# Kernel tuning notes

Hardware: AMD Instinct MI355X
Metric: run time of the kernel (lower is better)

## Reference

```python
import jax, jax.numpy as jnp
import numpy as np

BS, S, D, H, HS, HSEL, L = 32, 512, 512, 8, 2, 4, 6
DK = D // H  # 64
HD = H - HS  # dynamic heads


def setup_inputs() -> dict:
    key = jax.random.key(0)
    ks = jax.random.split(key, 10)
    w = lambda k, shape: jax.random.normal(k, shape, dtype=jnp.float32) * 0.02
    return {
        'q_embed_data': jax.random.normal(ks[0], (BS, S, D), jnp.float32),
        'qa_embed_data': jax.random.normal(ks[1], (BS, S, D), jnp.float32),
        # stacked per-layer params (torch Linear convention: W[out,in], y = x@W.T+b)
        'Wq': w(ks[2], (L, D, D)), 'bq': jnp.zeros((L, D), jnp.float32),
        'Wv': w(ks[3], (L, D, D)), 'bv': jnp.zeros((L, D), jnp.float32),
        'Wg': w(ks[4], (L, HD, D)),                      # routing gate, no bias
        'Wo': w(ks[5], (L, D, D)), 'bo': jnp.zeros((L, D), jnp.float32),
        'ln1_g': jnp.ones((L, D), jnp.float32), 'ln1_b': jnp.zeros((L, D), jnp.float32),
        'W1': w(ks[6], (L, D, D)), 'b1': jnp.zeros((L, D), jnp.float32),
        'W2': w(ks[7], (L, D, D)), 'b2': jnp.zeros((L, D), jnp.float32),
        'ln2_g': jnp.ones((L, D), jnp.float32), 'ln2_b': jnp.zeros((L, D), jnp.float32),
    }


def _layer_norm(x, g, b):
    m = x.mean(-1, keepdims=True)
    v = ((x - m) ** 2).mean(-1, keepdims=True)
    return (x - m) * jax.lax.rsqrt(v + 1e-5) * g + b


def _moh_attention(xq, xv, Wq, bq, Wv, bv, Wg, Wo, bo, strict):
    bs, s, d = xq.shape
    q = xq @ Wq.T + bq            # kq_same=True: k = q projection
    v = xv @ Wv.T + bv
    qh = q.reshape(bs, s, H, DK).transpose(0, 2, 1, 3)   # [b,h,s,dk]
    vh = v.reshape(bs, s, H, DK).transpose(0, 2, 1, 3)
    scores = jnp.einsum('bhqd,bhkd->bhqk', qh, qh) / jnp.sqrt(jnp.float32(DK))
    # mask==1 -> causal incl. diag; mask==0 -> strictly causal
    allow = jnp.tril(jnp.ones((s, s), bool), k=-1 if strict else 0)
    scores = jnp.where(allow, scores, jnp.float32(-1e9))
    # pad-zero shift: first query row replaced by zeros -> uniform attention
    scores = scores.at[:, :, 0, :].set(0.0)
    # per-token top-k head routing over dynamic heads
    gates = jax.nn.softmax(q.reshape(bs * s, D) @ Wg.T, axis=-1)  # [bs*s, HD]
    _, idx = jax.lax.top_k(gates, HSEL)
    dmask = jnp.zeros_like(gates).at[jnp.arange(bs * s)[:, None], idx].set(1.0)
    dyn = (gates * dmask).reshape(bs, s, HD)
    routing = jnp.concatenate([jnp.ones((bs, s, HS), gates.dtype), dyn], -1).mean(1)  # [b,H]
    attn = jax.nn.softmax(scores, axis=-1)
    ctx = jnp.einsum('bhqk,bhkd->bhqd', attn, vh) * routing[:, :, None, None]
    out = ctx.transpose(0, 2, 1, 3).reshape(bs, s, D) @ Wo.T + bo
    f = dmask.sum(0)
    P = gates.mean(0)
    balance = jnp.sum((f / (f.sum() + 1e-5)) * (P / (P.sum() + 1e-5)))
    return out, balance


def reference(q_embed_data, qa_embed_data, Wq, bq, Wv, bv, Wg, Wo, bo,
              ln1_g, ln1_b, W1, b1, W2, b2, ln2_g, ln2_b):
    def layer(i, xq, xv, strict):
        a, bl = _moh_attention(xq, xv, Wq[i], bq[i], Wv[i], bv[i], Wg[i], Wo[i], bo[i], strict)
        x = _layer_norm(xq + a, ln1_g[i], ln1_b[i])
        ffn = jax.nn.relu(x @ W1[i].T + b1[i]) @ W2[i].T + b2[i]
        return _layer_norm(x + ffn, ln2_g[i], ln2_b[i]), bl

    y = qa_embed_data
    x = q_embed_data
    # blocks_1: self-attention on y, mask=1
    y, _ = layer(0, y, y, False)
    y, _ = layer(1, y, y, False)
    # blocks_2: alternate mask=1 self-attn / mask=0 cross-attn (values=y)
    x, _ = layer(2, x, x, False)
    x, bl = layer(3, x, y, True)
    x, _ = layer(4, x, x, False)
    x, bl = layer(5, x, y, True)
    return (x, bl)
```

## Files before the change

kernel.cpp:

```cpp
#include <hip/hip_runtime.h>
#include <cstdint>

#define BSZ 32
#define SEQ 512
#define DM  512
#define NH  8
#define DK  64
#define HS_ 2
#define HD_ 6
#define NL  6
#define MROWS (BSZ*SEQ)
#define QVLD 1024
#define SCL 0.18033688011112043f

typedef unsigned short bf16_t;
typedef __attribute__((ext_vector_type(4))) float f32x4;
typedef __attribute__((ext_vector_type(8))) short bf16x8;
typedef __attribute__((ext_vector_type(8))) unsigned short u16x8;

#define DEV static __device__ __forceinline__

DEV float bf2f(bf16_t b) {
  unsigned int u = ((unsigned int)b) << 16;
  float f; __builtin_memcpy(&f, &u, 4); return f;
}
DEV bf16_t f2b(float f) {
  unsigned int u; __builtin_memcpy(&u, &f, 4);
  unsigned int r = (u + 0x7fffu + ((u >> 16) & 1u)) >> 16;
  return (bf16_t)r;
}
DEV void unp2(unsigned int w, float& a, float& b) {
  unsigned int ua = w << 16, ub = w & 0xffff0000u;
  __builtin_memcpy(&a, &ua, 4); __builtin_memcpy(&b, &ub, 4);
}
DEV unsigned cvtpk(float lo, float hi) {
  unsigned r;
  asm("v_cvt_pk_bf16_f32 %0, %1, %2" : "=v"(r) : "v"(lo), "v"(hi));
  return r;
}

DEV void gload_lds16(const bf16_t* g, bf16_t* l) {
  __builtin_amdgcn_global_load_lds(
      (const __attribute__((address_space(1))) void*)g,
      (__attribute__((address_space(3))) void*)l, 16, 0, 0);
}

DEV bf16x8 scale_q(bf16x8 v) {
  u16x8 u;
  __builtin_memcpy(&u, &v, 16);
  unsigned w[4];
#pragma unroll
  for (int e = 0; e < 4; ++e)
    w[e] = cvtpk(bf2f(u[2 * e]) * SCL, bf2f(u[2 * e + 1]) * SCL);
  bf16x8 r;
  __builtin_memcpy(&r, w, 16);
  return r;
}

__global__ __launch_bounds__(256) void f2b2_kernel(
    const float* __restrict__ s0, const float* __restrict__ s1,
    bf16_t* __restrict__ d0, bf16_t* __restrict__ d1) {
  const float* s = blockIdx.y ? s1 : s0;
  bf16_t* d = blockIdx.y ? d1 : d0;
  const int i = blockIdx.x * 256 + threadIdx.x;
  float4 v = reinterpret_cast<const float4*>(s)[i];
  ushort4 o;
  o.x = f2b(v.x); o.y = f2b(v.y); o.z = f2b(v.z); o.w = f2b(v.w);
  reinterpret_cast<ushort4*>(d)[i] = o;
}

__global__ __launch_bounds__(256) void f2bw_kernel(
    const float* __restrict__ s0, const float* __restrict__ s1,
    const float* __restrict__ s2, const float* __restrict__ s3,
    const float* __restrict__ s4, bf16_t* __restrict__ dst) {
  const float* srcs[5] = {s0, s1, s2, s3, s4};
  const float* s = srcs[blockIdx.y];
  bf16_t* d = dst + (size_t)blockIdx.y * ((size_t)NL * DM * DM);
  const int i = blockIdx.x * 256 + threadIdx.x;
  float4 v = reinterpret_cast<const float4*>(s)[i];
  ushort4 o;
  o.x = f2b(v.x); o.y = f2b(v.y); o.z = f2b(v.z); o.w = f2b(v.w);
  reinterpret_cast<ushort4*>(d)[i] = o;
}

__global__ __launch_bounds__(256) void gemm_qv(
    const bf16_t* __restrict__ A0, const bf16_t* __restrict__ A1,
    const bf16_t* __restrict__ W0, const bf16_t* __restrict__ W1,
    const float* __restrict__ b0, const float* __restrict__ b1,
    bf16_t* __restrict__ Yb) {
  const int K = 512;
  const int lin = blockIdx.y * 8 + blockIdx.x;
  const int swz = (lin & 7) * 128 + (lin >> 3);
  const int bn = swz & 7, bm = swz >> 3;
  const int tid = threadIdx.x, wid = tid >> 6, lane = tid & 63;
  const int wr = wid >> 1, wc = wid & 1;
  __shared__ __align__(16) bf16_t As[128 * 64];
  __shared__ __align__(16) bf16_t Bs[128 * 64];

  const bool hi = bn >= 4;
  const bf16_t* Asel = hi ? A1 : A0;
  const bf16_t* Wsel = hi ? (W1 - (size_t)512 * K) : W0;
  const float* bsel = hi ? (b1 - 512) : b0;

  f32x4 acc[4][4];
#pragma unroll
  for (int m = 0; m < 4; ++m)
#pragma unroll
    for (int n = 0; n < 4; ++n) acc[m][n] = f32x4{0.f, 0.f, 0.f, 0.f};

  const int lrow = lane & 15, lko = (lane >> 4) * 8;
  const int sr = wid * 8 + (lane >> 3), scol = (lane & 7) * 8;
  const size_t arow0 = (size_t)bm * 128, brow0 = (size_t)bn * 128;

  for (int k0 = 0; k0 < K; k0 += 64) {
#pragma unroll
    for (int i = 0; i < 4; ++i) {
      gload_lds16(Asel + (arow0 + i * 32 + sr) * K + k0 + scol, &As[(i * 4 + wid) * 512]);
      gload_lds16(Wsel + (brow0 + i * 32 + sr) * K + k0 + scol, &Bs[(i * 4 + wid) * 512]);
    }
    __syncthreads();
    bf16x8 af[4][2], bw[4][2];
#pragma unroll
    for (int m = 0; m < 4; ++m)
#pragma unroll
      for (int ks = 0; ks < 2; ++ks)
        af[m][ks] = *reinterpret_cast<const bf16x8*>(
            &As[(wr * 64 + m * 16 + lrow) * 64 + ks * 32 + lko]);
#pragma unroll
    for (int n = 0; n < 4; ++n)
#pragma unroll
      for (int ks = 0; ks < 2; ++ks)
        bw[n][ks] = *reinterpret_cast<const bf16x8*>(
            &Bs[(wc * 64 + n * 16 + lrow) * 64 + ks * 32 + lko]);
    __builtin_amdgcn_s_setprio(1);
#pragma unroll
    for (int ks = 0; ks < 2; ++ks)
#pragma unroll
      for (int m = 0; m < 4; ++m)
#pragma unroll
        for (int n = 0; n < 4; ++n)
          acc[m][n] = __builtin_amdgcn_mfma_f32_16x16x32_bf16(af[m][ks], bw[n][ks], acc[m][n], 0, 0, 0);
    __builtin_amdgcn_s_setprio(0);
    __syncthreads();
  }

  const int r0 = bm * 128 + wr * 64 + (lane >> 4) * 4;
  const int c0 = bn * 128 + wc * 64 + lrow;
#pragma unroll
  for (int n = 0; n < 4; ++n) {
    const int col = c0 + n * 16;
    const float bc = bsel[col];
#pragma unroll
    for (int m = 0; m < 4; ++m)
#pragma unroll
      for (int j = 0; j < 4; ++j)
        Yb[(size_t)(r0 + m * 16 + j) * QVLD + col] = f2b(acc[m][n][j] + bc);
  }
}

template <bool RELU>
__global__ __launch_bounds__(256) void gemm_n512(
    const bf16_t* __restrict__ A, const bf16_t* __restrict__ W,
    const float* __restrict__ bias, bf16_t* __restrict__ Yb) {
  const int K = 512;
  const int lin = blockIdx.y * 4 + blockIdx.x;
  const int swz = (lin & 7) * 128 + (lin >> 3);
  const int bn = swz & 3, bm = swz >> 2;
  const int tid = threadIdx.x, wid = tid >> 6, lane = tid & 63;
  const int wr = wid >> 1, wc = wid & 1;
  __shared__ __align__(16) bf16_t As[64 * 64];
  __shared__ __align__(16) bf16_t Bs[128 * 64];

  f32x4 acc[2][4];
#pragma unroll
  for (int m = 0; m < 2; ++m)
#pragma unroll
    for (int n = 0; n < 4; ++n) acc[m][n] = f32x4{0.f, 0.f, 0.f, 0.f};

  const int lrow = lane & 15, lko = (lane >> 4) * 8;
  const int sr = wid * 8 + (lane >> 3), scol = (lane & 7) * 8;
  const size_t arow0 = (size_t)bm * 64, brow0 = (size_t)bn * 128;

  for (int k0 = 0; k0 < K; k0 += 64) {
#pragma unroll
    for (int i = 0; i < 2; ++i)
      gload_lds16(A + (arow0 + i * 32 + sr) * K + k0 + scol, &As[(i * 4 + wid) * 512]);
#pragma unroll
    for (int i = 0; i < 4; ++i)
      gload_lds16(W + (brow0 + i * 32 + sr) * K + k0 + scol, &Bs[(i * 4 + wid) * 512]);
    __syncthreads();
    bf16x8 af[2][2], bw[4][2];
#pragma unroll
    for (int m = 0; m < 2; ++m)
#pragma unroll
      for (int ks = 0; ks < 2; ++ks)
        af[m][ks] = *reinterpret_cast<const bf16x8*>(
            &As[(wr * 32 + m * 16 + lrow) * 64 + ks * 32 + lko]);
#pragma unroll
    for (int n = 0; n < 4; ++n)
#pragma unroll
      for (int ks = 0; ks < 2; ++ks)
        bw[n][ks] = *reinterpret_cast<const bf16x8*>(
            &Bs[(wc * 64 + n * 16 + lrow) * 64 + ks * 32 + lko]);
    __builtin_amdgcn_s_setprio(1);
#pragma unroll
    for (int ks = 0; ks < 2; ++ks)
#pragma unroll
      for (int m = 0; m < 2; ++m)
#pragma unroll
        for (int n = 0; n < 4; ++n)
          acc[m][n] = __builtin_amdgcn_mfma_f32_16x16x32_bf16(af[m][ks], bw[n][ks], acc[m][n], 0, 0, 0);
    __builtin_amdgcn_s_setprio(0);
    __syncthreads();
  }

  const int r0 = bm * 64 + wr * 32 + (lane >> 4) * 4;
  const int c0 = bn * 128 + wc * 64 + lrow;
#pragma unroll
  for (int n = 0; n < 4; ++n) {
    const int col = c0 + n * 16;
    const float bc = bias[col];
#pragma unroll
    for (int m = 0; m < 2; ++m)
#pragma unroll
      for (int j = 0; j < 4; ++j) {
        float v = acc[m][n][j] + bc;
        if (RELU) v = fmaxf(v, 0.f);
        Yb[(size_t)(r0 + m * 16 + j) * DM + col] = f2b(v);
      }
  }
}

__global__ __launch_bounds__(256) void gates_kernel(
    const bf16_t* __restrict__ qv, const float* __restrict__ Wg,
    float* __restrict__ rdyn, float* __restrict__ fP) {
  __shared__ float wg_s[HD_ * DM];
  __shared__ float blk[4][18];
  const int tid = threadIdx.x, wid = tid >> 6, lane = tid & 63;
  for (int i = tid; i < HD_ * DM / 4; i += 256)
    reinterpret_cast<float4*>(wg_s)[i] = reinterpret_cast<const float4*>(Wg)[i];
  __syncthreads();
  const int bb = blockIdx.x >> 4;
  const int t0 = (blockIdx.x & 15) * 32 + wid * 8;
  float fs[6] = {0, 0, 0, 0, 0, 0}, ps[6] = {0, 0, 0, 0, 0, 0}, rs[6] = {0, 0, 0, 0, 0, 0};
  for (int it = 0; it < 8; ++it) {
    const int tok = bb * SEQ + t0 + it;
    uint4 u = reinterpret_cast<const uint4*>(qv + (size_t)tok * QVLD)[lane];
    float x[8];
    unp2(u.x, x[0], x[1]); unp2(u.y, x[2], x[3]);
    unp2(u.z, x[4], x[5]); unp2(u.w, x[6], x[7]);
    float g[6];
#pragma unroll
    for (int j = 0; j < 6; ++j) {
      float p = 0.f;
#pragma unroll
      for (int e = 0; e < 8; ++e) p = fmaf(x[e], wg_s[j * DM + lane * 8 + e], p);
#pragma unroll
      for (int off = 32; off; off >>= 1) p += __shfl_xor(p, off);
      g[j] = p;
    }
    float mx = g[0];
#pragma unroll
    for (int j = 1; j < 6; ++j) mx = fmaxf(mx, g[j]);
    float se = 0.f;
#pragma unroll
    for (int j = 0; j < 6; ++j) { g[j] = __expf(g[j] - mx); se += g[j]; }
    float inv = 1.f / se;
#pragma unroll
    for (int j = 0; j < 6; ++j) g[j] *= inv;
    int d1 = 0;
#pragma unroll
    for (int j = 1; j < 6; ++j)
      if (g[j] < g[d1] || (g[j] == g[d1] && j > d1)) d1 = j;
    int d2 = (d1 == 0) ? 1 : 0;
#pragma unroll
    for (int j = 0; j < 6; ++j) {
      if (j == d1) continue;
      if (g[j] < g[d2] || (g[j] == g[d2] && j > d2)) d2 = j;
    }
#pragma unroll
    for (int j = 0; j < 6; ++j) {
      const bool drop = (j == d1) || (j == d2);
      fs[j] += drop ? 0.f : 1.f;
      ps[j] += g[j];
      rs[j] += drop ? 0.f : g[j];
    }
  }
  if (lane == 0) {
#pragma unroll
    for (int j = 0; j < 6; ++j) {
      blk[wid][j] = fs[j]; blk[wid][6 + j] = ps[j]; blk[wid][12 + j] = rs[j];
    }
  }
  __syncthreads();
  if (tid < 18) {
    float s = blk[0][tid] + blk[1][tid] + blk[2][tid] + blk[3][tid];
    if (tid < 12) atomicAdd(&fP[tid], s);
    else atomicAdd(&rdyn[bb * 6 + (tid - 12)], s * (1.f / 512.f));
  }
}

__global__ __launch_bounds__(256, 2) void fattn_kernel(
    const bf16_t* __restrict__ qv, const float* __restrict__ rdyn,
    bf16_t* __restrict__ ctx, int strict) {
  const int bh = blockIdx.x, qt = blockIdx.y;
  const int b = bh >> 3, h = bh & 7;
  const int tid = threadIdx.x, wid = tid >> 6, lane = tid & 63;
  const int c0 = lane & 15, grp = lane >> 4;
  const int l3 = lane >> 3, c3 = lane & 7;
  const int kidx = lane & 31, dhalf = lane >> 5;

  __shared__ __align__(16) bf16_t Ks[64 * 64];
  __shared__ __align__(16) bf16_t Vt[64 * 72];
  __shared__ __align__(16) bf16_t Ps[4][32 * 64];
  __shared__ float csum[64];

  const bf16_t* qp = qv;
  const bf16_t* vp = qv + 512;
  const float factor = (h < HS_) ? 1.f : rdyn[b * 6 + (h - HS_)];

  const int qbase = qt * 128 + wid * 32;

  bf16x8 qf[2][2];
#pragma unroll
  for (int nt = 0; nt < 2; ++nt)
#pragma unroll
    for (int ks = 0; ks < 2; ++ks)
      qf[nt][ks] = scale_q(*reinterpret_cast<const bf16x8*>(
          qp + ((size_t)(b * SEQ + qbase + nt * 16 + c0)) * QVLD + h * DK + ks * 32 + grp * 8));

  f32x4 acc[2][4];
#pragma unroll
  for (int m = 0; m < 2; ++m)
#pragma unroll
    for (int d = 0; d < 4; ++d) acc[m][d] = f32x4{0.f, 0.f, 0.f, 0.f};
  float mreg[2] = {-3e38f, -3e38f};
  float lreg[2] = {0.f, 0.f};
  float cs[8] = {0, 0, 0, 0, 0, 0, 0, 0};

  const int lastk = (qbase + 31 - strict) >> 6;
  const int ktmax = 2 * qt + 1;

  for (int kt = 0; kt <= ktmax; ++kt) {
#pragma unroll
    for (int i = 0; i < 2; ++i) {
      int row = i * 32 + wid * 8 + l3;
      int blk = c3 ^ l3;
      gload_lds16(qp + ((size_t)(b * SEQ + kt * 64 + row)) * QVLD + h * DK + blk * 8,
                  Ks + (i * 32 + wid * 8) * 64);
    }
#pragma unroll
    for (int j = 0; j < 2; ++j) {
      const int d0 = (wid * 2 + j) * 8 + dhalf * 4;
      const bf16_t* src = vp + ((size_t)(b * SEQ + kt * 64 + 2 * kidx)) * QVLD + h * DK + d0;
      ushort4 lo = *reinterpret_cast<const ushort4*>(src);
      ushort4 hv = *reinterpret_cast<const ushort4*>(src + QVLD);
      *reinterpret_cast<unsigned*>(&Vt[(d0 + 0) * 72 + 2 * kidx]) = (unsigned)lo.x | ((unsigned)hv.x << 16);
      *reinterpret_cast<unsigned*>(&Vt[(d0 + 1) * 72 + 2 * kidx]) = (unsigned)lo.y | ((unsigned)hv.y << 16);
      *reinterpret_cast<unsigned*>(&Vt[(d0 + 2) * 72 + 2 * kidx]) = (unsigned)lo.z | ((unsigned)hv.z << 16);
      *reinterpret_cast<unsigned*>(&Vt[(d0 + 3) * 72 + 2 * kidx]) = (unsigned)lo.w | ((unsigned)hv.w << 16);
      if (qt == 3) {
        cs[j * 4 + 0] += bf2f(lo.x) + bf2f(hv.x);
        cs[j * 4 + 1] += bf2f(lo.y) + bf2f(hv.y);
        cs[j * 4 + 2] += bf2f(lo.z) + bf2f(hv.z);
        cs[j * 4 + 3] += bf2f(lo.w) + bf2f(hv.w);
      }
    }
    __syncthreads();

    if (kt <= lastk) {
      const char* KsB = (const char*)Ks;
      bf16x8 kf[4][2];
#pragma unroll
      for (int mt = 0; mt < 4; ++mt)
#pragma unroll
        for (int ks = 0; ks < 2; ++ks)
          kf[mt][ks] = *reinterpret_cast<const bf16x8*>(
              KsB + (mt * 16 + c0) * 128 + 16 * ((4 * ks + grp) ^ (c0 & 7)));
      f32x4 s[4][2];
#pragma unroll
      for (int mt = 0; mt < 4; ++mt)
#pragma unroll
        for (int nt = 0; nt < 2; ++nt) s[mt][nt] = f32x4{0.f, 0.f, 0.f, 0.f};
      __builtin_amdgcn_s_setprio(1);
#pragma unroll
      for (int mt = 0; mt < 4; ++mt)
#pragma unroll
        for (int nt = 0; nt < 2; ++nt)
#pragma unroll
          for (int ks = 0; ks < 2; ++ks)
            s[mt][nt] = __builtin_amdgcn_mfma_f32_16x16x32_bf16(
                kf[mt][ks], qf[nt][ks], s[mt][nt], 0, 0, 0);
      __builtin_amdgcn_s_setprio(0);

      const bool masked = (kt == lastk);
      if (masked) {
#pragma unroll
        for (int nt = 0; nt < 2; ++nt) {
          const int q = qbase + nt * 16 + c0;
#pragma unroll
          for (int mt = 0; mt < 4; ++mt)
#pragma unroll
            for (int j = 0; j < 4; ++j) {
              int k = kt * 64 + mt * 16 + grp * 4 + j;
              if (k + strict > q) s[mt][nt][j] = -1e30f;
            }
        }
      }
      float mx[2];
#pragma unroll
      for (int nt = 0; nt < 2; ++nt) {
        float a = fmaxf(s[0][nt][0], s[0][nt][1]);
        a = fmaxf(fmaxf(a, s[0][nt][2]), s[0][nt][3]);
        float bm_ = fmaxf(s[1][nt][0], s[1][nt][1]);
        bm_ = fmaxf(fmaxf(bm_, s[1][nt][2]), s[1][nt][3]);
        float c = fmaxf(s[2][nt][0], s[2][nt][1]);
        c = fmaxf(fmaxf(c, s[2][nt][2]), s[2][nt][3]);
        float d = fmaxf(s[3][nt][0], s[3][nt][1]);
        d = fmaxf(fmaxf(d, s[3][nt][2]), s[3][nt][3]);
        float m_ = fmaxf(fmaxf(a, bm_), fmaxf(c, d));
        m_ = fmaxf(m_, __shfl_xor(m_, 16));
        m_ = fmaxf(m_, __shfl_xor(m_, 32));
        mx[nt] = m_;
      }
      const bool defer = __all((mx[0] - mreg[0] <= 8.f) && (mx[1] - mreg[1] <= 8.f));
      float sc[2];
#pragma unroll
      for (int nt = 0; nt < 2; ++nt) {
        const float mnew = defer ? mreg[nt] : fmaxf(mreg[nt], mx[nt]);
        float ts = 0.f;
#pragma unroll
        for (int mt = 0; mt < 4; ++mt)
#pragma unroll
          for (int j = 0; j < 4; ++j) {
            float pp = exp2f(s[mt][nt][j] - mnew);
            s[mt][nt][j] = pp; ts += pp;
          }
        ts += __shfl_xor(ts, 16);
        ts += __shfl_xor(ts, 32);
        if (defer) {
          lreg[nt] += ts;
        } else {
          sc[nt] = exp2f(mreg[nt] - mnew);
          lreg[nt] = lreg[nt] * sc[nt] + ts;
          mreg[nt] = mnew;
        }
      }
      char* PsB = (char*)(&Ps[wid][0]);
#pragma unroll
      for (int nt = 0; nt < 2; ++nt)
#pragma unroll
        for (int mt = 0; mt < 4; ++mt) {
          uint2 w;
          w.x = cvtpk(s[mt][nt][0], s[mt][nt][1]);
          w.y = cvtpk(s[mt][nt][2], s[mt][nt][3]);
          int row = nt * 16 + c0;
          int off = (row * 128 + mt * 32 + grp * 8) ^ ((c0 & 7) << 4);
          *reinterpret_cast<uint2*>(PsB + off) = w;
        }
      if (!defer) {
#pragma unroll
        for (int mtq = 0; mtq < 2; ++mtq) {
          f32x4 sv;
#pragma unroll
          for (int j = 0; j < 4; ++j) sv[j] = __shfl(sc[mtq], grp * 4 + j);
#pragma unroll
          for (int dt = 0; dt < 4; ++dt) acc[mtq][dt] *= sv;
        }
      }
      bf16x8 pf[2][2], vf2[4][2];
#pragma unroll
      for (int mtq = 0; mtq < 2; ++mtq)
#pragma unroll
        for (int ks = 0; ks < 2; ++ks)
          pf[mtq][ks] = *reinterpret_cast<const bf16x8*>(
              PsB + (mtq * 16 + c0) * 128 + 16 * ((4 * ks + grp) ^ (c0 & 7)));
#pragma unroll
      for (int dt = 0; dt < 4; ++dt)
#pragma unroll
        for (int ks = 0; ks < 2; ++ks)
          vf2[dt][ks] = *reinterpret_cast<const bf16x8*>(
              (const char*)Vt + (dt * 16 + c0) * 144 + ks * 64 + grp * 16);
      __builtin_amdgcn_s_setprio(1);
#pragma unroll
      for (int mtq = 0; mtq < 2; ++mtq)
#pragma unroll
        for (int dt = 0; dt < 4; ++dt)
#pragma unroll
          for (int ks = 0; ks < 2; ++ks)
            acc[mtq][dt] = __builtin_amdgcn_mfma_f32_16x16x32_bf16(
                pf[mtq][ks], vf2[dt][ks], acc[mtq][dt], 0, 0, 0);
      __builtin_amdgcn_s_setprio(0);
    }
    __syncthreads();
  }

  if (qt == 3) {
#pragma unroll
    for (int e = 0; e < 8; ++e)
#pragma unroll
      for (int off = 1; off <= 16; off <<= 1) cs[e] += __shfl_xor(cs[e], off);
    if ((lane & 31) == 0) {
#pragma unroll
      for (int e = 0; e < 8; ++e)
        csum[(wid * 2 + (e >> 2)) * 8 + dhalf * 4 + (e & 3)] = cs[e];
    }
    __syncthreads();
    if (tid < 64)
      ctx[((size_t)(b * SEQ)) * DM + h * DK + tid] = f2b(csum[tid] * (1.f / 512.f) * factor);
  }

#pragma unroll
  for (int mtq = 0; mtq < 2; ++mtq) {
    const float inv = factor / lreg[mtq];
    f32x4 iv;
#pragma unroll
    for (int j = 0; j < 4; ++j) iv[j] = __shfl(inv, grp * 4 + j);
#pragma unroll
    for (int j = 0; j < 4; ++j) {
      const int q = qbase + mtq * 16 + grp * 4 + j;
      if (q == 0) continue;
#pragma unroll
      for (int dt = 0; dt < 4; ++dt)
        ctx[((size_t)(b * SEQ + q)) * DM + h * DK + dt * 16 + c0] =
            f2b(acc[mtq][dt][j] * iv[j]);
    }
  }
}

template <int OUT>
__global__ __launch_bounds__(256) void add_ln_kernel(
    const bf16_t* __restrict__ X, const bf16_t* __restrict__ A2,
    const float* __restrict__ gam, const float* __restrict__ bet,
    bf16_t* __restrict__ outb, float* __restrict__ outf) {
  const int wid = threadIdx.x >> 6, lane = threadIdx.x & 63;
  const size_t row = (size_t)blockIdx.x * 4 + wid;
  const size_t base = row * DM + lane * 8;
  uint4 xu = *reinterpret_cast<const uint4*>(X + base);
  uint4 au = *reinterpret_cast<const uint4*>(A2 + base);
  float z[8];
  {
    float p0, p1, q0, q1;
    unp2(xu.x, p0, p1); unp2(au.x, q0, q1); z[0] = p0 + q0; z[1] = p1 + q1;
    unp2(xu.y, p0, p1); unp2(au.y, q0, q1); z[2] = p0 + q0; z[3] = p1 + q1;
    unp2(xu.z, p0, p1); unp2(au.z, q0, q1); z[4] = p0 + q0; z[5] = p1 + q1;
    unp2(xu.w, p0, p1); unp2(au.w, q0, q1); z[6] = p0 + q0; z[7] = p1 + q1;
  }
  float s = 0.f;
#pragma unroll
  for (int e = 0; e < 8; ++e) s += z[e];
#pragma unroll
  for (int off = 32; off; off >>= 1) s += __shfl_xor(s, off);
  const float mean = s * (1.f / 512.f);
  float ss = 0.f;
#pragma unroll
  for (int e = 0; e < 8; ++e) { float d = z[e] - mean; ss += d * d; }
#pragma unroll
  for (int off = 32; off; off >>= 1) ss += __shfl_xor(ss, off);
  const float inv = rsqrtf(ss * (1.f / 512.f) + 1e-5f);
  float4 g0 = *reinterpret_cast<const float4*>(gam + lane * 8);
  float4 g1 = *reinterpret_cast<const float4*>(gam + lane * 8 + 4);
  float4 b0 = *reinterpret_cast<const float4*>(bet + lane * 8);
  float4 b1 = *reinterpret_cast<const float4*>(bet + lane * 8 + 4);
  float o[8];
  o[0] = (z[0] - mean) * inv * g0.x + b0.x;
  o[1] = (z[1] - mean) * inv * g0.y + b0.y;
  o[2] = (z[2] - mean) * inv * g0.z + b0.z;
  o[3] = (z[3] - mean) * inv * g0.w + b0.w;
  o[4] = (z[4] - mean) * inv * g1.x + b1.x;
  o[5] = (z[5] - mean) * inv * g1.y + b1.y;
  o[6] = (z[6] - mean) * inv * g1.z + b1.z;
  o[7] = (z[7] - mean) * inv * g1.w + b1.w;
  if (OUT == 0) {
    uint4 w;
    w.x = (unsigned)f2b(o[0]) | ((unsigned)f2b(o[1]) << 16);
    w.y = (unsigned)f2b(o[2]) | ((unsigned)f2b(o[3]) << 16);
    w.z = (unsigned)f2b(o[4]) | ((unsigned)f2b(o[5]) << 16);
    w.w = (unsigned)f2b(o[6]) | ((unsigned)f2b(o[7]) << 16);
    *reinterpret_cast<uint4*>(outb + base) = w;
  } else {
    float4 f0, f1;
    f0.x = o[0]; f0.y = o[1]; f0.z = o[2]; f0.w = o[3];
    f1.x = o[4]; f1.y = o[5]; f1.z = o[6]; f1.w = o[7];
    *reinterpret_cast<float4*>(outf + base) = f0;
    *reinterpret_cast<float4*>(outf + base + 4) = f1;
  }
}

__global__ void balance_kernel(const float* __restrict__ fP, float* __restrict__ out) {
  if (threadIdx.x == 0 && blockIdx.x == 0) {
    float fs = 0.f, pssum = 0.f, P[6];
    for (int j = 0; j < 6; ++j) {
      fs += fP[j];
      P[j] = fP[6 + j] * (1.f / (float)MROWS);
      pssum += P[j];
    }
    float bal = 0.f;
    for (int j = 0; j < 6; ++j)
      bal += (fP[j] / (fs + 1e-5f)) * (P[j] / (pssum + 1e-5f));
    out[0] = bal;
  }
}

extern "C" void kernel_launch(void* const* d_in, const int* in_sizes, int n_in,
                              void* d_out, int out_size, void* d_ws, size_t ws_size,
                              hipStream_t stream) {
  (void)in_sizes; (void)n_in; (void)out_size; (void)ws_size;
  const float* q_embed  = (const float*)d_in[0];
  const float* qa_embed = (const float*)d_in[1];
  const float* Wq  = (const float*)d_in[2];
  const float* bq  = (const float*)d_in[3];
  const float* Wv  = (const float*)d_in[4];
  const float* bv  = (const float*)d_in[5];
  const float* Wg  = (const float*)d_in[6];
  const float* Wo  = (const float*)d_in[7];
  const float* bo  = (const float*)d_in[8];
  const float* ln1g = (const float*)d_in[9];
  const float* ln1b = (const float*)d_in[10];
  const float* W1  = (const float*)d_in[11];
  const float* b1  = (const float*)d_in[12];
  const float* W2  = (const float*)d_in[13];
  const float* b2  = (const float*)d_in[14];
  const float* ln2g = (const float*)d_in[15];
  const float* ln2b = (const float*)d_in[16];

  char* p = (char*)d_ws;
  auto alloc = [&](size_t bytes) -> char* {
    char* r = p; p += (bytes + 255) & ~(size_t)255; return r;
  };
  const size_t WDE = (size_t)NL * DM * DM;
  const size_t AE  = (size_t)MROWS * DM;
  bf16_t* wall_b = (bf16_t*)alloc(5 * WDE * 2);
  bf16_t* wq_b = wall_b;
  bf16_t* wv_b = wall_b + WDE;
  bf16_t* wo_b = wall_b + 2 * WDE;
  bf16_t* w1_b = wall_b + 3 * WDE;
  bf16_t* w2_b = wall_b + 4 * WDE;
  bf16_t* y_b   = (bf16_t*)alloc(AE * 2);
  bf16_t* x_b   = (bf16_t*)alloc(AE * 2);
  bf16_t* qv_b  = (bf16_t*)alloc((size_t)MROWS * QVLD * 2);
  bf16_t* ctx_b = (bf16_t*)alloc(AE * 2);
  bf16_t* x1_b  = (bf16_t*)alloc(AE * 2);
  bf16_t* tmp_b = (bf16_t*)alloc(AE * 2);
  bf16_t* ffn1_b = (bf16_t*)alloc(AE * 2);
  float* stats = (float*)alloc(NL * (12 + BSZ * 6) * 4);
  float* fPbase = stats;
  float* rdynbase = stats + NL * 12;

  hipMemsetAsync(stats, 0, NL * (12 + BSZ * 6) * 4, stream);

  f2bw_kernel<<<dim3((unsigned)(WDE / 4 / 256), 5), 256, 0, stream>>>(
      Wq, Wv, Wo, W1, W2, wall_b);
  f2b2_kernel<<<dim3((unsigned)(AE / 4 / 256), 2), 256, 0, stream>>>(
      qa_embed, q_embed, y_b, x_b);

  const size_t DD = (size_t)DM * DM;
  dim3 gqv(8, 128), gn5(4, 256), gfa(256, 4);
  float* outx = (float*)d_out;

  auto layer = [&](int i, bf16_t* resb, const bf16_t* xvb, int strict, bool last) {
    float* fP = fPbase + i * 12;
    float* rdyn = rdynbase + i * (BSZ * 6);
    gemm_qv<<<gqv, 256, 0, stream>>>(
        resb, xvb, wq_b + i * DD, wv_b + i * DD, bq + i * DM, bv + i * DM, qv_b);
    gates_kernel<<<MROWS / 32, 256, 0, stream>>>(qv_b, Wg + (size_t)i * HD_ * DM, rdyn, fP);
    fattn_kernel<<<gfa, 256, 0, stream>>>(qv_b, rdyn, ctx_b, strict);
    gemm_n512<false><<<gn5, 256, 0, stream>>>(ctx_b, wo_b + i * DD, bo + i * DM, tmp_b);
    add_ln_kernel<0><<<MROWS / 4, 256, 0, stream>>>(
        resb, tmp_b, ln1g + i * DM, ln1b + i * DM, x1_b, nullptr);
    gemm_n512<true><<<gn5, 256, 0, stream>>>(x1_b, w1_b + i * DD, b1 + i * DM, ffn1_b);
    gemm_n512<false><<<gn5, 256, 0, stream>>>(ffn1_b, w2_b + i * DD, b2 + i * DM, tmp_b);
    if (last)
      add_ln_kernel<1><<<MROWS / 4, 256, 0, stream>>>(
          x1_b, tmp_b, ln2g + i * DM, ln2b + i * DM, nullptr, outx);
    else
      add_ln_kernel<0><<<MROWS / 4, 256, 0, stream>>>(
          x1_b, tmp_b, ln2g + i * DM, ln2b + i * DM, resb, nullptr);
  };

  layer(0, y_b, y_b, 0, false);
  layer(1, y_b, y_b, 0, false);
  layer(2, x_b, x_b, 0, false);
  layer(3, x_b, y_b, 1, false);
  layer(4, x_b, x_b, 0, false);
  layer(5, x_b, y_b, 1, true);
  balance_kernel<<<1, 64, 0, stream>>>(fPbase + 5 * 12, outx + (size_t)MROWS * DM);
}
```

Before: 969.3 us.

## Replace GEMMs with unified 8-wave 128x256 triple-buffered pipelined kernel

Replaces the QV projection GEMM and the 512-wide GEMMs with one templated kernel. It uses 512 threads, 128x256 output tiles, a three-stage LDS ring buffer with an XOR swizzle, and explicit vmcnt waits and barriers, so global loads overlap with the MFMA work. Larger tiles raise operand reuse and reduce the block count. In exchange it uses 144KB of shared memory, which limits occupancy to one block per CU, and it relies on hand-managed wait counts that are easy to get wrong.

```diff
diff --git a/kernel.cpp b/kernel.cpp
--- a/kernel.cpp
+++ b/kernel.cpp
@@ -83,21 +83,25 @@
   reinterpret_cast<ushort4*>(d)[i] = o;
 }
 
-__global__ __launch_bounds__(256) void gemm_qv(
+template <int NB, int NWG, bool RELU>
+__global__ __launch_bounds__(512) void gemm8(
     const bf16_t* __restrict__ A0, const bf16_t* __restrict__ A1,
     const bf16_t* __restrict__ W0, const bf16_t* __restrict__ W1,
     const float* __restrict__ b0, const float* __restrict__ b1,
-    bf16_t* __restrict__ Yb) {
+    bf16_t* __restrict__ Yb, int ldy) {
   const int K = 512;
-  const int lin = blockIdx.y * 8 + blockIdx.x;
-  const int swz = (lin & 7) * 128 + (lin >> 3);
-  const int bn = swz & 7, bm = swz >> 3;
+  const int lin = blockIdx.y * NB + blockIdx.x;
+  const int cpx = NWG / 8;
+  const int swz = (lin & 7) * cpx + (lin >> 3);
+  const int bn = swz % NB, bm = swz / NB;
   const int tid = threadIdx.x, wid = tid >> 6, lane = tid & 63;
-  const int wr = wid >> 1, wc = wid & 1;
-  __shared__ __align__(16) bf16_t As[128 * 64];
-  __shared__ __align__(16) bf16_t Bs[128 * 64];
-
-  const bool hi = bn >= 4;
+  const int wr = wid >> 2, wc = wid & 3;
+  const int lrow = lane & 15, grp = lane >> 4;
+  const int l3 = lane >> 3, c3 = lane & 7;
+
+  __shared__ __align__(16) bf16_t Lds[3][24576];
+
+  const bool hi = (bn * 256) >= 512;
   const bf16_t* Asel = hi ? A1 : A0;
   const bf16_t* Wsel = hi ? (W1 - (size_t)512 * K) : W0;
   const float* bsel = hi ? (b1 - 512) : b0;
@@ -108,125 +112,102 @@
 #pragma unroll
     for (int n = 0; n < 4; ++n) acc[m][n] = f32x4{0.f, 0.f, 0.f, 0.f};
 
-  const int lrow = lane & 15, lko = (lane >> 4) * 8;
-  const int sr = wid * 8 + (lane >> 3), scol = (lane & 7) * 8;
-  const size_t arow0 = (size_t)bm * 128, brow0 = (size_t)bn * 128;
-
-  for (int k0 = 0; k0 < K; k0 += 64) {
-#pragma unroll
-    for (int i = 0; i < 4; ++i) {
-      gload_lds16(Asel + (arow0 + i * 32 + sr) * K + k0 + scol, &As[(i * 4 + wid) * 512]);
-      gload_lds16(Wsel + (brow0 + i * 32 + sr) * K + k0 + scol, &Bs[(i * 4 + wid) * 512]);
-    }
-    __syncthreads();
-    bf16x8 af[4][2], bw[4][2];
-#pragma unroll
-    for (int m = 0; m < 4; ++m)
+  const char* LB = (const char*)Lds;
+
+  auto stage3 = [&](int kt, int buf, int half) {
+#pragma unroll
+    for (int cc = 0; cc < 3; ++cc) {
+      const int c = wid + (half * 3 + cc) * 8;
+      const int colb = ((c3 ^ l3) * 8);
+      if (c < 16) {
+        gload_lds16(Asel + (size_t)(bm * 128 + c * 8 + l3) * K + kt * 64 + colb,
+                    &Lds[buf][c * 512]);
+      } else {
+        const int cb = c - 16;
+        gload_lds16(Wsel + (size_t)(bn * 256 + cb * 8 + l3) * K + kt * 64 + colb,
+                    &Lds[buf][8192 + cb * 512]);
+      }
+    }
+  };
+  auto rdA = [&](int buf, int rA, int ks) -> bf16x8 {
+    const int off = buf * 49152 + rA * 128 + ((ks * 64 + grp * 16) ^ ((rA & 7) << 4));
+    return *reinterpret_cast<const bf16x8*>(LB + off);
+  };
+  auto rdB = [&](int buf, int rB, int ks) -> bf16x8 {
+    const int off = buf * 49152 + 16384 + rB * 128 + ((ks * 64 + grp * 16) ^ ((rB & 7) << 4));
+    return *reinterpret_cast<const bf16x8*>(LB + off);
+  };
+
+  stage3(0, 0, 0); stage3(0, 0, 1);
+  stage3(1, 1, 0); stage3(1, 1, 1);
+  asm volatile("s_waitcnt vmcnt(6)" ::: "memory");
+  __builtin_amdgcn_s_barrier();
+
+  for (int g = 0; g < 8; ++g) {
+    const int bufR = g % 3, bufW = (g + 2) % 3;
+    const bool st = g < 6;
+    bf16x8 bwv[4][2], afv[2][2];
+#pragma unroll
+    for (int n = 0; n < 4; ++n)
 #pragma unroll
       for (int ks = 0; ks < 2; ++ks)
-        af[m][ks] = *reinterpret_cast<const bf16x8*>(
-            &As[(wr * 64 + m * 16 + lrow) * 64 + ks * 32 + lko]);
-#pragma unroll
-    for (int n = 0; n < 4; ++n)
+        bwv[n][ks] = rdB(bufR, wc * 64 + n * 16 + lrow, ks);
+#pragma unroll
+    for (int m = 0; m < 2; ++m)
 #pragma unroll
       for (int ks = 0; ks < 2; ++ks)
-        bw[n][ks] = *reinterpret_cast<const bf16x8*>(
-            &Bs[(wc * 64 + n * 16 + lrow) * 64 + ks * 32 + lko]);
+        afv[m][ks] = rdA(bufR, wr * 64 + m * 16 + lrow, ks);
+    if (st) stage3(g + 2, bufW, 0);
+    __builtin_amdgcn_s_barrier();
+    asm volatile("s_waitcnt lgkmcnt(0)" ::: "memory");
     __builtin_amdgcn_s_setprio(1);
 #pragma unroll
     for (int ks = 0; ks < 2; ++ks)
 #pragma unroll
-      for (int m = 0; m < 4; ++m)
+      for (int m = 0; m < 2; ++m)
 #pragma unroll
         for (int n = 0; n < 4; ++n)
-          acc[m][n] = __builtin_amdgcn_mfma_f32_16x16x32_bf16(af[m][ks], bw[n][ks], acc[m][n], 0, 0, 0);
+          acc[m][n] = __builtin_amdgcn_mfma_f32_16x16x32_bf16(afv[m][ks], bwv[n][ks], acc[m][n], 0, 0, 0);
     __builtin_amdgcn_s_setprio(0);
-    __syncthreads();
-  }
-
-  const int r0 = bm * 128 + wr * 64 + (lane >> 4) * 4;
-  const int c0 = bn * 128 + wc * 64 + lrow;
+    __builtin_amdgcn_s_barrier();
+#pragma unroll
+    for (int m = 0; m < 2; ++m)
+#pragma unroll
+      for (int ks = 0; ks < 2; ++ks)
+        afv[m][ks] = rdA(bufR, wr * 64 + 32 + m * 16 + lrow, ks);
+    if (st) stage3(g + 2, bufW, 1);
+    __builtin_amdgcn_s_barrier();
+    asm volatile("s_waitcnt lgkmcnt(0)" ::: "memory");
+    __builtin_amdgcn_s_setprio(1);
+#pragma unroll
+    for (int ks = 0; ks < 2; ++ks)
+#pragma unroll
+      for (int m = 0; m < 2; ++m)
+#pragma unroll
+        for (int n = 0; n < 4; ++n)
+          acc[2 + m][n] = __builtin_amdgcn_mfma_f32_16x16x32_bf16(afv[m][ks], bwv[n][ks], acc[2 + m][n], 0, 0, 0);
+    __builtin_amdgcn_s_setprio(0);
+    if (g < 6) {
+      asm volatile("s_waitcnt vmcnt(6)" ::: "memory");
+    } else if (g == 6) {
+      asm volatile("s_waitcnt vmcnt(0)" ::: "memory");
+    }
+    __builtin_amdgcn_s_barrier();
+  }
+
+  const int r0 = bm * 128 + wr * 64 + grp * 4;
+  const int c0 = bn * 256 + wc * 64 + lrow;
 #pragma unroll
   for (int n = 0; n < 4; ++n) {
     const int col = c0 + n * 16;
     const float bc = bsel[col];
 #pragma unroll
-    for (int m = 0; m < 4; ++m)
-#pragma unroll
-      for (int j = 0; j < 4; ++j)
-        Yb[(size_t)(r0 + m * 16 + j) * QVLD + col] = f2b(acc[m][n][j] + bc);
-  }
-}
-
-template <bool RELU>
-__global__ __launch_bounds__(256) void gemm_n512(
-    const bf16_t* __restrict__ A, const bf16_t* __restrict__ W,
-    const float* __restrict__ bias, bf16_t* __restrict__ Yb) {
-  const int K = 512;
-  const int lin = blockIdx.y * 4 + blockIdx.x;
-  const int swz = (lin & 7) * 128 + (lin >> 3);
-  const int bn = swz & 3, bm = swz >> 2;
-  const int tid = threadIdx.x, wid = tid >> 6, lane = tid & 63;
-  const int wr = wid >> 1, wc = wid & 1;
-  __shared__ __align__(16) bf16_t As[64 * 64];
-  __shared__ __align__(16) bf16_t Bs[128 * 64];
-
-  f32x4 acc[2][4];
-#pragma unroll
-  for (int m = 0; m < 2; ++m)
-#pragma unroll
-    for (int n = 0; n < 4; ++n) acc[m][n] = f32x4{0.f, 0.f, 0.f, 0.f};
-
-  const int lrow = lane & 15, lko = (lane >> 4) * 8;
-  const int sr = wid * 8 + (lane >> 3), scol = (lane & 7) * 8;
-  const size_t arow0 = (size_t)bm * 64, brow0 = (size_t)bn * 128;
-
-  for (int k0 = 0; k0 < K; k0 += 64) {
-#pragma unroll
-    for (int i = 0; i < 2; ++i)
-      gload_lds16(A + (arow0 + i * 32 + sr) * K + k0 + scol, &As[(i * 4 + wid) * 512]);
-#pragma unroll
-    for (int i = 0; i < 4; ++i)
-      gload_lds16(W + (brow0 + i * 32 + sr) * K + k0 + scol, &Bs[(i * 4 + wid) * 512]);
-    __syncthreads();
-    bf16x8 af[2][2], bw[4][2];
-#pragma unroll
-    for (int m = 0; m < 2; ++m)
-#pragma unroll
-      for (int ks = 0; ks < 2; ++ks)
-        af[m][ks] = *reinterpret_cast<const bf16x8*>(
-            &As[(wr * 32 + m * 16 + lrow) * 64 + ks * 32 + lko]);
-#pragma unroll
-    for (int n = 0; n < 4; ++n)
-#pragma unroll
-      for (int ks = 0; ks < 2; ++ks)
-        bw[n][ks] = *reinterpret_cast<const bf16x8*>(
-            &Bs[(wc * 64 + n * 16 + lrow) * 64 + ks * 32 + lko]);
-    __builtin_amdgcn_s_setprio(1);
-#pragma unroll
-    for (int ks = 0; ks < 2; ++ks)
-#pragma unroll
-      for (int m = 0; m < 2; ++m)
-#pragma unroll
-        for (int n = 0; n < 4; ++n)
-          acc[m][n] = __builtin_amdgcn_mfma_f32_16x16x32_bf16(af[m][ks], bw[n][ks], acc[m][n], 0, 0, 0);
-    __builtin_amdgcn_s_setprio(0);
-    __syncthreads();
-  }
-
-  const int r0 = bm * 64 + wr * 32 + (lane >> 4) * 4;
-  const int c0 = bn * 128 + wc * 64 + lrow;
-#pragma unroll
-  for (int n = 0; n < 4; ++n) {
-    const int col = c0 + n * 16;
-    const float bc = bias[col];
-#pragma unroll
-    for (int m = 0; m < 2; ++m)
+    for (int qm = 0; qm < 4; ++qm)
 #pragma unroll
       for (int j = 0; j < 4; ++j) {
-        float v = acc[m][n][j] + bc;
+        float v = acc[qm][n][j] + bc;
         if (RELU) v = fmaxf(v, 0.f);
-        Yb[(size_t)(r0 + m * 16 + j) * DM + col] = f2b(v);
+        Yb[(size_t)(r0 + qm * 16 + j) * ldy + col] = f2b(v);
       }
   }
 }
@@ -655,21 +636,24 @@
       qa_embed, q_embed, y_b, x_b);
 
   const size_t DD = (size_t)DM * DM;
-  dim3 gqv(8, 128), gn5(4, 256), gfa(256, 4);
+  dim3 gqv(4, 128), gn5(2, 128), gfa(256, 4);
   float* outx = (float*)d_out;
 
   auto layer = [&](int i, bf16_t* resb, const bf16_t* xvb, int strict, bool last) {
     float* fP = fPbase + i * 12;
     float* rdyn = rdynbase + i * (BSZ * 6);
-    gemm_qv<<<gqv, 256, 0, stream>>>(
-        resb, xvb, wq_b + i * DD, wv_b + i * DD, bq + i * DM, bv + i * DM, qv_b);
+    gemm8<4, 512, false><<<gqv, 512, 0, stream>>>(
+        resb, xvb, wq_b + i * DD, wv_b + i * DD, bq + i * DM, bv + i * DM, qv_b, QVLD);
     gates_kernel<<<MROWS / 32, 256, 0, stream>>>(qv_b, Wg + (size_t)i * HD_ * DM, rdyn, fP);
     fattn_kernel<<<gfa, 256, 0, stream>>>(qv_b, rdyn, ctx_b, strict);
-    gemm_n512<false><<<gn5, 256, 0, stream>>>(ctx_b, wo_b + i * DD, bo + i * DM, tmp_b);
+    gemm8<2, 256, false><<<gn5, 512, 0, stream>>>(
+        ctx_b, ctx_b, wo_b + i * DD, wo_b + i * DD, bo + i * DM, bo + i * DM, tmp_b, DM);
     add_ln_kernel<0><<<MROWS / 4, 256, 0, stream>>>(
         resb, tmp_b, ln1g + i * DM, ln1b + i * DM, x1_b, nullptr);
-    gemm_n512<true><<<gn5, 256, 0, stream>>>(x1_b, w1_b + i * DD, b1 + i * DM, ffn1_b);
-    gemm_n512<false><<<gn5, 256, 0, stream>>>(ffn1_b, w2_b + i * DD, b2 + i * DM, tmp_b);
+    gemm8<2, 256, true><<<gn5, 512, 0, stream>>>(
+        x1_b, x1_b, w1_b + i * DD, w1_b + i * DD, b1 + i * DM, b1 + i * DM, ffn1_b, DM);
+    gemm8<2, 256, false><<<gn5, 512, 0, stream>>>(
+        ffn1_b, ffn1_b, w2_b + i * DD, w2_b + i * DD, b2 + i * DM, b2 + i * DM, tmp_b, DM);
     if (last)
       add_ln_kernel<1><<<MROWS / 4, 256, 0, stream>>>(
           x1_b, tmp_b, ln2g + i * DM, ln2b + i * DM, nullptr, outx);
```

Result: faster. 899.9 us (-7.2%).
